# Optimization experiments

Measured on AMD Instinct MI355X. Metric: run time of the kernel, lower is better.

Reference implementation:

```python
import jax, jax.numpy as jnp
import numpy as np

CONF_W, POS_W, LEN_W, TRIG_W, CONST_W = 1.0, 1.0, 0.1, 1.0, 0.5
FOCAL_THR = 0.1
EPS = 6e-08


def setup_inputs() -> dict:
    key = jax.random.key(0)
    k1, k2, k3, k4, k5 = jax.random.split(key, 5)
    B, C, H, W = 32, 10, 192, 320
    u = jax.random.uniform(k1, (B, H, W), dtype=jnp.float32)
    gt0 = jnp.where(u > 0.95, 1.0, u * 2.0 - 1.0)
    gt_rest = jax.random.normal(k2, (B, C - 1, H, W), dtype=jnp.float32) * 0.5
    gt = jnp.concatenate([gt0[:, None], gt_rest], axis=1)
    # re channel 0: confidence strictly in (0,1) so logs are finite
    re0 = jax.random.uniform(k3, (B, 1, H, W), dtype=jnp.float32, minval=0.05, maxval=0.95)
    re_rest = jax.random.normal(k4, (B, C - 1, H, W), dtype=jnp.float32) * 0.5
    re = jnp.concatenate([re0, re_rest], axis=1)
    return {"re": re, "gt": gt}


def _smooth_l1(d):
    ad = jnp.abs(d)
    return jnp.where(ad < 1.0, 0.5 * d * d, ad - 0.5)


def _forward(re, gt):
    gt0 = gt[:, 0]  # [B,H,W]
    re0 = re[:, 0]
    m0 = gt0 >= 0.0            # confidence mask (above 0)
    mv = gt0 == 1.0            # vehicle mask
    m0f = m0.astype(jnp.float32)
    mvf = mv.astype(jnp.float32)
    nv = mvf.sum()             # number of vehicle pixels (one channel)

    def mse2(rc, gc):
        # mean over two masked channels
        s = sum(((re[:, r] - gt[:, g]) ** 2 * mvf).sum() for r, g in zip(rc, gc))
        return s / (2.0 * nv)

    def sl1_2(rc, gc):
        s = sum((_smooth_l1(re[:, r] - gt[:, g]) * mvf).sum() for r, g in zip(rc, gc))
        return s / (2.0 * nv)

    # focal confidence loss (threshold 0.1) over pixels with gt0 >= 0
    pos = m0f * (gt0 >= FOCAL_THR).astype(jnp.float32)
    neg = m0f * (gt0 < FOCAL_THR).astype(jnp.float32)
    num_pos = pos.sum()
    safe_re = jnp.clip(re0, 1e-6, 1.0 - 1e-6)  # masked-out entries must not NaN
    pos_term = -(pos * (gt0 - re0) ** 2 * jnp.log(safe_re + EPS)).sum()
    neg_term = -(neg * re0 ** 2 * jnp.log(1.0 + EPS - safe_re) * (1.0 - gt0) ** 4).sum()
    focal = jnp.where(num_pos == 0.0, neg_term, (pos_term + neg_term) / num_pos)

    confidence_loss = CONF_W * focal
    pos_loss = POS_W * sl1_2([1, 2], [1, 2])
    length_v1 = LEN_W * sl1_2([3, 6], [3, 6])
    length_v2 = LEN_W * sl1_2([3, 6], [6, 3])
    trig_v1 = TRIG_W * (mse2([4, 7], [4, 7]) + mse2([5, 8], [5, 8]))
    trig_v2 = TRIG_W * (mse2([4, 7], [7, 4]) + mse2([5, 8], [8, 5]))

    const1 = (((1.0 - re[:, 5] ** 2 - re[:, 4] ** 2) ** 2) * mvf).sum() / nv
    const2 = (((1.0 - re[:, 8] ** 2 - re[:, 7] ** 2) ** 2) * mvf).sum() / nv
    const_loss = CONST_W * (const1 + const2)

    height_loss = LEN_W * (_smooth_l1(re[:, 9] - gt[:, 9]) * mvf).sum() / nv

    dimensions_loss = jnp.minimum(length_v1 + trig_v1, length_v2 + trig_v2) + height_loss
    return confidence_loss + pos_loss + dimensions_loss + const_loss


def reference(re, gt):
    return _forward(re, gt)
```

## Files before the change

### kernel.cpp

```cpp
#include <hip/hip_runtime.h>
#include <math.h>

constexpr int B_ = 32, C_ = 10, H_ = 192, W_ = 320;
constexpr int HW_  = H_ * W_;
constexpr int CHW_ = C_ * HW_;
constexpr int NPTS = B_ * HW_;
constexpr int NV4  = NPTS / 4;
constexpr int NBLK = NV4 / 256;

#define NACC 11
#define PAD  32

__device__ __forceinline__ float sl1f(float d) {
    float ad = fabsf(d);
    return ad < 1.0f ? 0.5f * d * d : ad - 0.5f;
}

__global__ __launch_bounds__(256) void loss_main(
    const float* __restrict__ re, const float* __restrict__ gt,
    float* __restrict__ ws)
{
    const int tid = blockIdx.x * 256 + threadIdx.x;
    float acc[NACC];
#pragma unroll
    for (int i = 0; i < NACC; ++i) acc[i] = 0.0f;

    if (tid < NV4) {
        const int p = tid * 4;
        const int b = p / HW_;
        const int s = p - b * HW_;
        const float* rp = re + (size_t)b * CHW_ + s;
        const float* gp = gt + (size_t)b * CHW_ + s;

        const float4 g4 = *(const float4*)gp;
        const float4 r4 = *(const float4*)rp;
        float gv[4] = {g4.x, g4.y, g4.z, g4.w};
        float rv[4] = {r4.x, r4.y, r4.z, r4.w};
        float mv[4];
        float any = 0.0f;

#pragma unroll
        for (int j = 0; j < 4; ++j) {
            const float g = gv[j], r = rv[j];
            const float m = (g == 1.0f) ? 1.0f : 0.0f;
            mv[j] = m; any += m;
            acc[0] += m;
            const float pos = (g >= 0.1f) ? 1.0f : 0.0f;
            const float neg = ((g >= 0.0f) && (g < 0.1f)) ? 1.0f : 0.0f;
            acc[1] += pos;
            const float safe = fminf(fmaxf(r, 1e-6f), 1.0f - 1e-6f);
            const float d = g - r;
            acc[2] += pos * (d * d) * logf(safe + 6e-8f);
            const float omg = 1.0f - g;
            const float omg2 = omg * omg;
            acc[3] += neg * (r * r) * logf(1.0f + 6e-8f - safe) * (omg2 * omg2);
        }

        if (any != 0.0f) {
            float rc[9][4], gc[9][4];
#pragma unroll
            for (int c = 0; c < 9; ++c) {
                const float4 t = *(const float4*)(rp + (c + 1) * HW_);
                rc[c][0] = t.x; rc[c][1] = t.y; rc[c][2] = t.z; rc[c][3] = t.w;
                const float4 u = *(const float4*)(gp + (c + 1) * HW_);
                gc[c][0] = u.x; gc[c][1] = u.y; gc[c][2] = u.z; gc[c][3] = u.w;
            }
#pragma unroll
            for (int j = 0; j < 4; ++j) {
                const float m = mv[j];
                const float r1 = rc[0][j], r2 = rc[1][j], r3 = rc[2][j];
                const float r4v = rc[3][j], r5 = rc[4][j], r6 = rc[5][j];
                const float r7 = rc[6][j], r8 = rc[7][j], r9 = rc[8][j];
                const float g1 = gc[0][j], g2 = gc[1][j], g3 = gc[2][j];
                const float g4v = gc[3][j], g5 = gc[4][j], g6 = gc[5][j];
                const float g7 = gc[6][j], g8 = gc[7][j], g9 = gc[8][j];

                acc[4] += m * (sl1f(r1 - g1) + sl1f(r2 - g2));
                acc[5] += m * (sl1f(r3 - g3) + sl1f(r6 - g6));
                acc[6] += m * (sl1f(r3 - g6) + sl1f(r6 - g3));
                const float d44 = r4v - g4v, d77 = r7 - g7;
                const float d55 = r5 - g5,  d88 = r8 - g8;
                acc[7] += m * (d44 * d44 + d77 * d77 + d55 * d55 + d88 * d88);
                const float d47 = r4v - g7, d74 = r7 - g4v;
                const float d58 = r5 - g8,  d85 = r8 - g5;
                acc[8] += m * (d47 * d47 + d74 * d74 + d58 * d58 + d85 * d85);
                const float c1 = 1.0f - r5 * r5 - r4v * r4v;
                const float c2 = 1.0f - r8 * r8 - r7 * r7;
                acc[9] += m * (c1 * c1 + c2 * c2);
                acc[10] += m * sl1f(r9 - g9);
            }
        }
    }

    __shared__ float smem[NACC][4];
    const int lane = threadIdx.x & 63;
    const int wid  = threadIdx.x >> 6;
#pragma unroll
    for (int i = 0; i < NACC; ++i) {
        float v = acc[i];
#pragma unroll
        for (int off = 32; off > 0; off >>= 1) v += __shfl_down(v, off, 64);
        if (lane == 0) smem[i][wid] = v;
    }
    __syncthreads();
    if (threadIdx.x < NACC) {
        const int i = threadIdx.x;
        const float v = smem[i][0] + smem[i][1] + smem[i][2] + smem[i][3];
        atomicAdd(&ws[i * PAD], v);
    }
}

__global__ void loss_finalize(const float* __restrict__ ws, float* __restrict__ out)
{
    const float nv     = ws[0 * PAD];
    const float npos   = ws[1 * PAD];
    const float pterm  = -ws[2 * PAD];
    const float nterm  = -ws[3 * PAD];
    const float focal  = (npos == 0.0f) ? nterm : (pterm + nterm) / npos;

    const float inv2nv = 1.0f / (2.0f * nv);
    const float invnv  = 1.0f / nv;

    const float pos_loss = 1.0f * ws[4 * PAD] * inv2nv;
    const float lv1      = 0.1f * ws[5 * PAD] * inv2nv;
    const float lv2      = 0.1f * ws[6 * PAD] * inv2nv;
    const float tv1      = 1.0f * ws[7 * PAD] * inv2nv;
    const float tv2      = 1.0f * ws[8 * PAD] * inv2nv;
    const float cl       = 0.5f * ws[9 * PAD] * invnv;
    const float hl       = 0.1f * ws[10 * PAD] * invnv;

    const float dims = fminf(lv1 + tv1, lv2 + tv2) + hl;
    out[0] = 1.0f * focal + pos_loss + dims + cl;
}

extern "C" void kernel_launch(void* const* d_in, const int* in_sizes, int n_in,
                              void* d_out, int out_size, void* d_ws, size_t ws_size,
                              hipStream_t stream)
{
    const float* re = (const float*)d_in[0];
    const float* gt = (const float*)d_in[1];
    float* ws  = (float*)d_ws;
    float* out = (float*)d_out;

    hipMemsetAsync(d_ws, 0, NACC * PAD * sizeof(float), stream);
    loss_main<<<NBLK, 256, 0, stream>>>(re, gt, ws);
    loss_finalize<<<1, 1, 0, stream>>>(ws, out);
}
```

Baseline: 176.3 us.

## Replace global atomics with per-block partials and a single-block reduce kernel

Each block now writes its 11 partial sums to its own workspace slots instead of doing atomicAdd on shared counters, and a 256-thread reduce kernel sums the partials and computes the final loss. This removes the memset launch and the atomic contention on 11 addresses across about 1920 blocks. It also drops the tid<NV4 bounds check, which is safe because NV4 divides evenly by 256, and adds an occupancy hint to launch_bounds. In exchange, the second kernel does more work than the old single-thread finalize, which adds some tail latency.

Measured after the change: 197.4 us. 1.12x slower.

```diff
diff --git a/kernel.cpp b/kernel.cpp
--- a/kernel.cpp
+++ b/kernel.cpp
@@ -9,14 +9,13 @@
 constexpr int NBLK = NV4 / 256;
 
 #define NACC 11
-#define PAD  32
 
 __device__ __forceinline__ float sl1f(float d) {
     float ad = fabsf(d);
     return ad < 1.0f ? 0.5f * d * d : ad - 0.5f;
 }
 
-__global__ __launch_bounds__(256) void loss_main(
+__global__ __launch_bounds__(256, 4) void loss_main(
     const float* __restrict__ re, const float* __restrict__ gt,
     float* __restrict__ ws)
 {
@@ -25,7 +24,7 @@
 #pragma unroll
     for (int i = 0; i < NACC; ++i) acc[i] = 0.0f;
 
-    if (tid < NV4) {
+    {
         const int p = tid * 4;
         const int b = p / HW_;
         const int s = p - b * HW_;
@@ -105,32 +104,53 @@
     __syncthreads();
     if (threadIdx.x < NACC) {
         const int i = threadIdx.x;
-        const float v = smem[i][0] + smem[i][1] + smem[i][2] + smem[i][3];
-        atomicAdd(&ws[i * PAD], v);
+        ws[i * NBLK + blockIdx.x] =
+            smem[i][0] + smem[i][1] + smem[i][2] + smem[i][3];
     }
 }
 
-__global__ void loss_finalize(const float* __restrict__ ws, float* __restrict__ out)
+__global__ __launch_bounds__(256) void loss_reduce(
+    const float* __restrict__ ws, float* __restrict__ out)
 {
-    const float nv     = ws[0 * PAD];
-    const float npos   = ws[1 * PAD];
-    const float pterm  = -ws[2 * PAD];
-    const float nterm  = -ws[3 * PAD];
-    const float focal  = (npos == 0.0f) ? nterm : (pterm + nterm) / npos;
+    __shared__ float slot_sum[NACC];
+    __shared__ float smem[4];
+    const int lane = threadIdx.x & 63;
+    const int wid  = threadIdx.x >> 6;
 
-    const float inv2nv = 1.0f / (2.0f * nv);
-    const float invnv  = 1.0f / nv;
+    for (int i = 0; i < NACC; ++i) {
+        float v = 0.0f;
+        for (int b = threadIdx.x; b < NBLK; b += 256)
+            v += ws[i * NBLK + b];
+#pragma unroll
+        for (int off = 32; off > 0; off >>= 1) v += __shfl_down(v, off, 64);
+        if (lane == 0) smem[wid] = v;
+        __syncthreads();
+        if (threadIdx.x == 0)
+            slot_sum[i] = smem[0] + smem[1] + smem[2] + smem[3];
+        __syncthreads();
+    }
 
-    const float pos_loss = 1.0f * ws[4 * PAD] * inv2nv;
-    const float lv1      = 0.1f * ws[5 * PAD] * inv2nv;
-    const float lv2      = 0.1f * ws[6 * PAD] * inv2nv;
-    const float tv1      = 1.0f * ws[7 * PAD] * inv2nv;
-    const float tv2      = 1.0f * ws[8 * PAD] * inv2nv;
-    const float cl       = 0.5f * ws[9 * PAD] * invnv;
-    const float hl       = 0.1f * ws[10 * PAD] * invnv;
+    if (threadIdx.x == 0) {
+        const float nv     = slot_sum[0];
+        const float npos   = slot_sum[1];
+        const float pterm  = -slot_sum[2];
+        const float nterm  = -slot_sum[3];
+        const float focal  = (npos == 0.0f) ? nterm : (pterm + nterm) / npos;
 
-    const float dims = fminf(lv1 + tv1, lv2 + tv2) + hl;
-    out[0] = 1.0f * focal + pos_loss + dims + cl;
+        const float inv2nv = 1.0f / (2.0f * nv);
+        const float invnv  = 1.0f / nv;
+
+        const float pos_loss = 1.0f * slot_sum[4] * inv2nv;
+        const float lv1      = 0.1f * slot_sum[5] * inv2nv;
+        const float lv2      = 0.1f * slot_sum[6] * inv2nv;
+        const float tv1      = 1.0f * slot_sum[7] * inv2nv;
+        const float tv2      = 1.0f * slot_sum[8] * inv2nv;
+        const float cl       = 0.5f * slot_sum[9] * invnv;
+        const float hl       = 0.1f * slot_sum[10] * invnv;
+
+        const float dims = fminf(lv1 + tv1, lv2 + tv2) + hl;
+        out[0] = 1.0f * focal + pos_loss + dims + cl;
+    }
 }
 
 extern "C" void kernel_launch(void* const* d_in, const int* in_sizes, int n_in,
@@ -142,7 +162,6 @@
     float* ws  = (float*)d_ws;
     float* out = (float*)d_out;
 
-    hipMemsetAsync(d_ws, 0, NACC * PAD * sizeof(float), stream);
     loss_main<<<NBLK, 256, 0, stream>>>(re, gt, ws);
-    loss_finalize<<<1, 1, 0, stream>>>(ws, out);
+    loss_reduce<<<1, 256, 0, stream>>>(ws, out);
 }
```
